# Kernel tuning notes

Hardware: AMD Instinct MI355X
Metric: run time of the kernel (lower is better)

The kernel has to match this reference:

```python
import jax, jax.numpy as jnp
import numpy as np

N = 100000      # nodes
E = 1600000     # edges
IN_DIM = 128    # node_feat_dim
HID = 64        # hidden_dim
K = 3           # Chebyshev order
LAMBDA_MAX = 2.0  # PyG ChebConv default for 'sym' normalization


def setup_inputs():
    key = jax.random.key(0)
    ks = jax.random.split(key, 11)
    x = jax.random.normal(ks[0], (N, IN_DIM), jnp.float32)
    edge_index = jax.random.randint(ks[1], (2, E), 0, N)
    edge_weight = jax.random.uniform(ks[2], (E,), jnp.float32)
    h = jax.random.normal(ks[3], (N, HID), jnp.float32)
    c = jax.random.normal(ks[4], (N, HID), jnp.float32)
    s_in = 1.0 / np.sqrt(IN_DIM)
    s_h = 1.0 / np.sqrt(HID)
    # stacked gate params, order: [input, forget, cell(candidate), output]
    Wx = jax.random.uniform(ks[5], (4, IN_DIM, HID), jnp.float32, -s_in, s_in)
    bg = jax.random.uniform(ks[6], (4, HID), jnp.float32, -s_h, s_h)
    theta = jax.random.uniform(ks[7], (4, K, HID, HID), jnp.float32, -s_h, s_h)
    conv_b = jax.random.uniform(ks[8], (4, HID), jnp.float32, -s_h, s_h)
    Wl = jax.random.uniform(ks[9], (HID, HID), jnp.float32, -s_h, s_h)
    bl = jax.random.uniform(ks[10], (HID,), jnp.float32, -s_h, s_h)
    return dict(x=x, edge_index=edge_index, edge_weight=edge_weight, h=h, c=c,
                Wx=Wx, bg=bg, theta=theta, conv_b=conv_b, Wl=Wl, bl=bl)


def _make_lhat_mm(edge_index, edge_weight, num_nodes, lambda_max):
    # Builds z -> L_hat @ z  with  L_hat = (2/lambda_max) * (I - D^-1/2 A D^-1/2) - I
    src, dst = edge_index[0], edge_index[1]
    w = jnp.where(src == dst, 0.0, edge_weight)  # remove_self_loops
    deg = jax.ops.segment_sum(w, src, num_segments=num_nodes)
    deg_safe = jnp.where(deg > 0, deg, 1.0)
    dinv = jnp.where(deg > 0, jax.lax.rsqrt(deg_safe), 0.0)  # inf -> 0 as in PyG
    lap_w = (2.0 / lambda_max) * (-dinv[src] * w * dinv[dst])  # scaled off-diagonal
    diag = 2.0 / lambda_max - 1.0                              # scaled diag (0 at lmax=2)
    def lhat_mm(z):
        msg = lap_w[:, None] * z[src]                       # [E, HID] gather
        agg = jax.ops.segment_sum(msg, dst, num_segments=num_nodes)
        return agg + diag * z
    return lhat_mm


def reference(x, edge_index, edge_weight, h, c, Wx, bg, theta, conv_b, Wl, bl):
    lhat_mm = _make_lhat_mm(edge_index, edge_weight, x.shape[0], LAMBDA_MAX)
    # Chebyshev basis T_k(L_hat) h ; identical across the 4 gate ChebConvs, so compute once.
    Tx = [h, lhat_mm(h)]
    for _ in range(2, K):
        Tx.append(2.0 * lhat_mm(Tx[-1]) - Tx[-2])
    Tx = jnp.stack(Tx)                                      # [K, N, HID]
    conv = jnp.einsum('knh,gkho->gno', Tx, theta) + conv_b[:, None, :]
    lin = jnp.einsum('nf,gfo->gno', x, Wx) + bg[:, None, :]
    pre = lin + conv                                        # [4, N, HID]
    i = jax.nn.sigmoid(pre[0])
    f = jax.nn.sigmoid(pre[1])
    t = jnp.tanh(pre[2])
    o = jax.nn.sigmoid(pre[3])
    c0 = f * c + i * t
    h0 = o * jnp.tanh(c0)
    out = jax.nn.relu(h0) @ Wl + bl                         # trailing relu + Linear
    return (out, h0, c0)
```

## Files before the change

kernel.cpp:

```cpp
#include <hip/hip_runtime.h>
#include <hip/hip_bf16.h>

#define NN 100000
#define NE 1600000
#define INDIM 128
#define HID 64
#define BSH 9
#define NBUCK 196

typedef __hip_bfloat16 bf16;
typedef unsigned short ushort;
typedef unsigned int uint;
typedef __attribute__((ext_vector_type(8))) short short8;
typedef __attribute__((ext_vector_type(4))) float floatx4;

__device__ __forceinline__ float b2f(bf16 v) { return __bfloat162float(v); }
__device__ __forceinline__ float b2f_raw(ushort u) { return __uint_as_float(((uint)u) << 16); }
__device__ __forceinline__ ushort f2bu(float v) {
    bf16 t = __float2bfloat16(v);
    return *reinterpret_cast<ushort*>(&t);
}
__device__ __forceinline__ float ldin(const void* p, int i, int f32) {
    return f32 ? ((const float*)p)[i] : b2f(((const bf16*)p)[i]);
}
__device__ __forceinline__ float sigmoidf(float x) { return 1.f / (1.f + __expf(-x)); }
__device__ __forceinline__ float tanh_fast(float x) {
    float e = __expf(2.f * x);
    return 1.f - 2.f / (e + 1.f);
}
__device__ __forceinline__ uint4 packf8(const float* f) {
    uint4 u;
    u.x = f2bu(f[0]) | ((uint)f2bu(f[1]) << 16);
    u.y = f2bu(f[2]) | ((uint)f2bu(f[3]) << 16);
    u.z = f2bu(f[4]) | ((uint)f2bu(f[5]) << 16);
    u.w = f2bu(f[6]) | ((uint)f2bu(f[7]) << 16);
    return u;
}
__device__ __forceinline__ uint4 ld8_bf16(const void* p, int off, int f32) {
    if (!f32) return *(const uint4*)((const ushort*)p + off);
    const float* q = (const float*)p + off;
    float4 a = *(const float4*)q, b = *(const float4*)(q + 4);
    float f[8] = {a.x, a.y, a.z, a.w, b.x, b.y, b.z, b.w};
    return packf8(f);
}
__device__ __forceinline__ void ld4w(const void* ew, int e0, int f32, float* w) {
    if (f32) {
        float4 v = *(const float4*)((const float*)ew + e0);
        w[0] = v.x; w[1] = v.y; w[2] = v.z; w[3] = v.w;
    } else {
        uint2 v = *(const uint2*)((const ushort*)ew + e0);
        w[0] = b2f_raw((ushort)(v.x & 0xffff)); w[1] = b2f_raw((ushort)(v.x >> 16));
        w[2] = b2f_raw((ushort)(v.y & 0xffff)); w[3] = b2f_raw((ushort)(v.y >> 16));
    }
}

__global__ void k_sniff(const void* __restrict__ x, int* __restrict__ flag) {
    __shared__ int cnt;
    if (threadIdx.x == 0) cnt = 0;
    __syncthreads();
    const bf16* p = (const bf16*)x;
    int bad = 0;
    for (int i = threadIdx.x; i < 8192; i += 256) {
        float v = b2f(p[i]);
        if (!(fabsf(v) < 1e6f)) bad++;
    }
    atomicAdd(&cnt, bad);
    __syncthreads();
    if (threadIdx.x == 0) flag[0] = (cnt > 32) ? 1 : 0;
}

__global__ __launch_bounds__(256)
void k_count(const int* __restrict__ ei, int* __restrict__ gcntD,
             int* __restrict__ gcntS) {
    __shared__ int hD[NBUCK], hS[NBUCK];
    for (int i = threadIdx.x; i < NBUCK; i += 256) { hD[i] = 0; hS[i] = 0; }
    __syncthreads();
    int e0 = (blockIdx.x * 256 + threadIdx.x) * 16;
    if (e0 < NE) {
        if (e0 + 16 <= NE) {
#pragma unroll
            for (int q = 0; q < 4; q++) {
                int4 s4 = *(const int4*)(ei + e0 + q * 4);
                int4 d4 = *(const int4*)(ei + NE + e0 + q * 4);
                int ss[4] = {s4.x, s4.y, s4.z, s4.w};
                int dd[4] = {d4.x, d4.y, d4.z, d4.w};
#pragma unroll
                for (int j = 0; j < 4; j++)
                    if (ss[j] != dd[j]) {
                        atomicAdd(hD + (dd[j] >> BSH), 1);
                        atomicAdd(hS + (ss[j] >> BSH), 1);
                    }
            }
        } else {
            for (int e = e0; e < NE; e++) {
                int s = ei[e], d = ei[NE + e];
                if (s != d) {
                    atomicAdd(hD + (d >> BSH), 1);
                    atomicAdd(hS + (s >> BSH), 1);
                }
            }
        }
    }
    __syncthreads();
    for (int i = threadIdx.x; i < NBUCK; i += 256) {
        if (hD[i]) atomicAdd(gcntD + i, hD[i]);
        if (hS[i]) atomicAdd(gcntS + i, hS[i]);
    }
}

__global__ __launch_bounds__(256)
void k_scanb(const int* __restrict__ gcntD, const int* __restrict__ gcntS,
             int* __restrict__ bbaseD, int* __restrict__ bbaseS,
             int* __restrict__ gcurD, int* __restrict__ gcurS,
             int* __restrict__ rowptr) {
    __shared__ int sh[256];
    const int t = threadIdx.x;
    int v = (t < NBUCK) ? gcntD[t] : 0;
    sh[t] = v; __syncthreads();
    for (int off = 1; off < 256; off <<= 1) {
        int u = (t >= off) ? sh[t - off] : 0;
        __syncthreads(); sh[t] += u; __syncthreads();
    }
    if (t < NBUCK) { int e = sh[t] - v; bbaseD[t] = e; gcurD[t] = e; }
    if (t == 255) { bbaseD[NBUCK] = sh[255]; rowptr[NN] = sh[255]; }
    __syncthreads();
    int v2 = (t < NBUCK) ? gcntS[t] : 0;
    sh[t] = v2; __syncthreads();
    for (int off = 1; off < 256; off <<= 1) {
        int u = (t >= off) ? sh[t - off] : 0;
        __syncthreads(); sh[t] += u; __syncthreads();
    }
    if (t < NBUCK) { int e = sh[t] - v2; bbaseS[t] = e; gcurS[t] = e; }
    if (t == 255) bbaseS[NBUCK] = sh[255];
}

__global__ __launch_bounds__(256)
void k_part(const int* __restrict__ ei, const void* __restrict__ ew,
            int* __restrict__ gcurD, int* __restrict__ gcurS,
            int2* __restrict__ recD, int2* __restrict__ recS,
            const int* __restrict__ flagp) {
    const int f32 = flagp[0];
    __shared__ int cD[NBUCK], cS[NBUCK], bD[NBUCK], bS[NBUCK];
    for (int i = threadIdx.x; i < NBUCK; i += 256) { cD[i] = 0; cS[i] = 0; }
    __syncthreads();
    const int e0 = (blockIdx.x * 256 + threadIdx.x) * 8;
    int s[8], d[8], rD[8], rS[8];
    float w[8];
    bool act[8];
    if (e0 + 8 <= NE) {
        int4 sa = *(const int4*)(ei + e0), sb = *(const int4*)(ei + e0 + 4);
        int4 da = *(const int4*)(ei + NE + e0), db = *(const int4*)(ei + NE + e0 + 4);
        s[0]=sa.x; s[1]=sa.y; s[2]=sa.z; s[3]=sa.w;
        s[4]=sb.x; s[5]=sb.y; s[6]=sb.z; s[7]=sb.w;
        d[0]=da.x; d[1]=da.y; d[2]=da.z; d[3]=da.w;
        d[4]=db.x; d[5]=db.y; d[6]=db.z; d[7]=db.w;
        ld4w(ew, e0, f32, w); ld4w(ew, e0 + 4, f32, w + 4);
#pragma unroll
        for (int j = 0; j < 8; j++) act[j] = (s[j] != d[j]);
    } else {
#pragma unroll
        for (int j = 0; j < 8; j++) {
            int e = e0 + j;
            if (e < NE) {
                s[j] = ei[e]; d[j] = ei[NE + e]; w[j] = ldin(ew, e, f32);
                act[j] = (s[j] != d[j]);
            } else { s[j] = 0; d[j] = 0; w[j] = 0.f; act[j] = false; }
        }
    }
#pragma unroll
    for (int j = 0; j < 8; j++)
        if (act[j]) {
            rD[j] = atomicAdd(cD + (d[j] >> BSH), 1);
            rS[j] = atomicAdd(cS + (s[j] >> BSH), 1);
        }
    __syncthreads();
    for (int i = threadIdx.x; i < NBUCK; i += 256) {
        bD[i] = cD[i] ? atomicAdd(gcurD + i, cD[i]) : 0;
        bS[i] = cS[i] ? atomicAdd(gcurS + i, cS[i]) : 0;
    }
    __syncthreads();
#pragma unroll
    for (int j = 0; j < 8; j++)
        if (act[j]) {
            int2 pd; pd.x = s[j] | ((d[j] & 511) << 17); pd.y = __float_as_int(w[j]);
            recD[bD[d[j] >> BSH] + rD[j]] = pd;
            int2 ps; ps.x = s[j] & 511; ps.y = __float_as_int(w[j]);
            recS[bS[s[j] >> BSH] + rS[j]] = ps;
        }
}

__global__ __launch_bounds__(512)
void k_build(const int2* __restrict__ recD, const int2* __restrict__ recS,
             const int* __restrict__ bbaseD, const int* __restrict__ bbaseS,
             int* __restrict__ rowptr, int2* __restrict__ csr,
             float* __restrict__ dinv) {
    __shared__ int cnt[512], sh[512], cur[512];
    __shared__ float degf[512];
    const int t = threadIdx.x, b = blockIdx.x;
    cnt[t] = 0; degf[t] = 0.f;
    __syncthreads();
    const int dbase = bbaseD[b], dend = bbaseD[b + 1];
    const int sbase = bbaseS[b], send = bbaseS[b + 1];
    const int nD = dend - dbase, nS = send - sbase;
    const int2* rd = recD + dbase;
    const int2* rs = recS + sbase;
    for (int i = t; i < nD; i += 512) atomicAdd(cnt + (rd[i].x >> 17), 1);
    for (int i = t; i < nS; i += 512) atomicAdd(degf + rs[i].x, __int_as_float(rs[i].y));
    __syncthreads();
    const int own = cnt[t];
    sh[t] = own; __syncthreads();
    for (int off = 1; off < 512; off <<= 1) {
        int u = (t >= off) ? sh[t - off] : 0;
        __syncthreads(); sh[t] += u; __syncthreads();
    }
    const int rstart = dbase + sh[t] - own;
    cur[t] = rstart;
    const int node = (b << BSH) + t;
    if (node < NN) {
        rowptr[node] = rstart;
        float dg = degf[t];
        dinv[node] = dg > 0.f ? rsqrtf(dg) : 0.f;
    }
    __syncthreads();
    for (int i = t; i < nD; i += 512) {
        int2 r = rd[i];
        int pos = atomicAdd(cur + (r.x >> 17), 1);
        int2 o; o.x = r.x & 0x1FFFF; o.y = r.y;
        csr[pos] = o;
    }
}

template<int MODE>
__global__ __launch_bounds__(256)
void k_gath(const int* __restrict__ rowptr, const float* __restrict__ dinv,
            const int2* __restrict__ csr, const void* __restrict__ zin,
            void* __restrict__ outv, const int* __restrict__ flagp) {
    const int f32 = flagp[0];
    int n = (blockIdx.x * 256 + threadIdx.x) >> 6;
    int lane = threadIdx.x & 63;
    if (n >= NN) return;
    int b0 = rowptr[n], e0 = rowptr[n + 1];
    const int2* row = csr + b0;
    int cnt = e0 - b0;
    float acc = 0.f;
    int i = 0;
#define ZLD(sidx) (MODE == 0 ? ldin(zin, (sidx) * 64 + lane, f32) \
                             : b2f_raw(((const ushort*)zin)[(sidx) * 128 + lane]))
    for (; i + 3 < cnt; i += 4) {
        int2 p0 = row[i], p1 = row[i + 1], p2 = row[i + 2], p3 = row[i + 3];
        float z0 = ZLD(p0.x), z1 = ZLD(p1.x), z2 = ZLD(p2.x), z3 = ZLD(p3.x);
        acc = fmaf(dinv[p0.x] * __int_as_float(p0.y), z0, acc);
        acc = fmaf(dinv[p1.x] * __int_as_float(p1.y), z1, acc);
        acc = fmaf(dinv[p2.x] * __int_as_float(p2.y), z2, acc);
        acc = fmaf(dinv[p3.x] * __int_as_float(p3.y), z3, acc);
    }
    for (; i < cnt; i++) {
        int2 p0 = row[i];
        float z0 = ZLD(p0.x);
        acc = fmaf(dinv[p0.x] * __int_as_float(p0.y), z0, acc);
    }
#undef ZLD
    float r = -dinv[n] * acc;
    if (MODE == 0) ((ushort*)outv)[(size_t)n * 128 + lane] = f2bu(r);
    else           ((float*)outv)[(size_t)n * 64 + lane] = r;
}

__global__ void k_wcat(const void* __restrict__ Wx, const void* __restrict__ theta,
                       const void* __restrict__ bg, const void* __restrict__ convb,
                       const void* __restrict__ Wl,
                       ushort* __restrict__ Wf, float* __restrict__ biasP,
                       ushort* __restrict__ WlF, const int* __restrict__ flagp) {
    const int f32 = flagp[0];
    int gid = blockIdx.x * 256 + threadIdx.x;
    if (gid < 81920) {
        int j = gid & 7, l = (gid >> 3) & 63, tile = gid >> 9;
        int kc = tile >> 4, t = tile & 15;
        int r = kc * 32 + ((l >> 4) * 8) + j;
        int g = t & 3;
        int cc = (t >> 2) * 16 + (l & 15);
        float v;
        if (r < 128) {
            v = ldin(Wx, (g * 128 + r) * 64 + cc, f32);
        } else {
            int k3 = (r - 128) >> 6, rr = (r - 128) & 63;
            v = ldin(theta, ((g * 3 + k3) * 64 + rr) * 64 + cc, f32);
        }
        Wf[gid] = f2bu(v);
        if (gid < 256) {
            int o = gid;
            int gg = (o >> 4) & 3;
            int cc2 = (o >> 6) * 16 + (o & 15);
            biasP[o] = ldin(bg, gg * 64 + cc2, f32) + ldin(convb, gg * 64 + cc2, f32);
        }
    } else {
        int gid2 = gid - 81920;
        int j = gid2 & 7, l = (gid2 >> 3) & 63, tile2 = gid2 >> 9;
        int kc2 = tile2 >> 2, t = tile2 & 3;
        int k = kc2 * 32 + ((l >> 4) * 8) + j;
        int n = t * 16 + (l & 15);
        WlF[gid2] = f2bu(ldin(Wl, k * 64 + n, f32));
    }
}

__global__ __launch_bounds__(256)
void k_gates(const void* __restrict__ x, const void* __restrict__ h,
             const void* __restrict__ cin,
             const ushort* __restrict__ Tx1, const float* __restrict__ agg2,
             const ushort* __restrict__ Wf, const float* __restrict__ biasP,
             const ushort* __restrict__ WlF, const void* __restrict__ bl,
             float* __restrict__ outF, float* __restrict__ h0o,
             float* __restrict__ c0o, const int* __restrict__ flagp) {
    const int f32 = flagp[0];
    __shared__ ushort As[4 * 64 * 8];
    __shared__ ushort Hs[64 * 72];
    const int tid = threadIdx.x;
    const int lane = tid & 63;
    const int w = tid >> 6;
    const int base = blockIdx.x * 64;
    const int sm = tid & 63;
    const int skq = tid >> 6;
    const int snode = base + sm;
    const bool svalid = snode < NN;
    uint4* sdst = (uint4*)&As[(((sm >> 4) * 64) + ((sm & 15) + 16 * skq)) * 8];

    floatx4 acc[4][4];
    {
        float bv0 = biasP[w * 64 + 0 * 16 + (lane & 15)];
        float bv1 = biasP[w * 64 + 1 * 16 + (lane & 15)];
        float bv2 = biasP[w * 64 + 2 * 16 + (lane & 15)];
        float bv3 = biasP[w * 64 + 3 * 16 + (lane & 15)];
#pragma unroll
        for (int mt = 0; mt < 4; mt++) {
            acc[mt][0] = (floatx4){bv0, bv0, bv0, bv0};
            acc[mt][1] = (floatx4){bv1, bv1, bv1, bv1};
            acc[mt][2] = (floatx4){bv2, bv2, bv2, bv2};
            acc[mt][3] = (floatx4){bv3, bv3, bv3, bv3};
        }
    }

    for (int kc = 0; kc < 10; kc++) {
        uint4 raw = {0, 0, 0, 0};
        if (svalid) {
            if (kc < 4) {
                raw = ld8_bf16(x, snode * 128 + kc * 32 + skq * 8, f32);
            } else if (kc < 6) {
                raw = ld8_bf16(h, snode * 64 + (kc - 4) * 32 + skq * 8, f32);
            } else if (kc < 8) {
                raw = *(const uint4*)&Tx1[(size_t)snode * 128 + (kc - 6) * 32 + skq * 8];
            } else {
                int off = snode * 64 + (kc - 8) * 32 + skq * 8;
                const float* pa = agg2 + off;
                float4 a = *(const float4*)pa, b = *(const float4*)(pa + 4);
                float av[8] = {a.x, a.y, a.z, a.w, b.x, b.y, b.z, b.w};
                float hv[8];
                if (f32) {
                    const float* ph = (const float*)h + off;
                    float4 h0_ = *(const float4*)ph, h1_ = *(const float4*)(ph + 4);
                    hv[0]=h0_.x; hv[1]=h0_.y; hv[2]=h0_.z; hv[3]=h0_.w;
                    hv[4]=h1_.x; hv[5]=h1_.y; hv[6]=h1_.z; hv[7]=h1_.w;
                } else {
                    uint4 hr = *(const uint4*)((const ushort*)h + off);
                    uint u[4] = {hr.x, hr.y, hr.z, hr.w};
#pragma unroll
                    for (int q = 0; q < 4; q++) {
                        hv[2*q]   = b2f_raw((ushort)(u[q] & 0xffff));
                        hv[2*q+1] = b2f_raw((ushort)(u[q] >> 16));
                    }
                }
                float f[8];
#pragma unroll
                for (int j = 0; j < 8; j++) f[j] = 2.f * av[j] - hv[j];
                raw = packf8(f);
            }
        }
        short8 bF[4];
#pragma unroll
        for (int g = 0; g < 4; g++)
            bF[g] = *(const short8*)&Wf[((kc * 16 + w * 4 + g) * 64 + lane) * 8];

        __syncthreads();
        *sdst = raw;
        __syncthreads();

        short8 aF[4];
#pragma unroll
        for (int mt = 0; mt < 4; mt++)
            aF[mt] = *(const short8*)&As[(mt * 64 + lane) * 8];
#pragma unroll
        for (int mt = 0; mt < 4; mt++)
#pragma unroll
            for (int g = 0; g < 4; g++)
                acc[mt][g] = __builtin_amdgcn_mfma_f32_16x16x32_bf16(
                    aF[mt], bF[g], acc[mt][g], 0, 0, 0);
    }

    const int cc = w * 16 + (lane & 15);
#pragma unroll
    for (int mt = 0; mt < 4; mt++) {
        const int m0 = mt * 16 + ((lane >> 4) * 4);
#pragma unroll
        for (int r = 0; r < 4; r++) {
            int ml = m0 + r;
            int node = base + ml;
            float gi = sigmoidf(acc[mt][0][r]);
            float gf = sigmoidf(acc[mt][1][r]);
            float gt = tanh_fast(acc[mt][2][r]);
            float go = sigmoidf(acc[mt][3][r]);
            float cv = (node < NN) ? ldin(cin, node * 64 + cc, f32) : 0.f;
            float c0 = gf * cv + gi * gt;
            float h0v = go * tanh_fast(c0);
            if (node < NN) {
                c0o[node * 64 + cc] = c0;
                h0o[node * 64 + cc] = h0v;
            }
            Hs[ml * 72 + cc] = f2bu(fmaxf(h0v, 0.f));
        }
    }
    __syncthreads();

    float blv = ldin(bl, w * 16 + (lane & 15), f32);
    floatx4 oacc[4];
#pragma unroll
    for (int mt = 0; mt < 4; mt++) oacc[mt] = (floatx4){blv, blv, blv, blv};
#pragma unroll
    for (int kc2 = 0; kc2 < 2; kc2++) {
        short8 bW = *(const short8*)&WlF[((kc2 * 4 + w) * 64 + lane) * 8];
#pragma unroll
        for (int mt = 0; mt < 4; mt++) {
            short8 aH = *(const short8*)&Hs[(mt * 16 + (lane & 15)) * 72
                                            + kc2 * 32 + (lane >> 4) * 8];
            oacc[mt] = __builtin_amdgcn_mfma_f32_16x16x32_bf16(
                aH, bW, oacc[mt], 0, 0, 0);
        }
    }
#pragma unroll
    for (int mt = 0; mt < 4; mt++) {
        const int m0 = mt * 16 + ((lane >> 4) * 4);
#pragma unroll
        for (int r = 0; r < 4; r++) {
            int node = base + m0 + r;
            if (node < NN)
                outF[node * 64 + w * 16 + (lane & 15)] = oacc[mt][r];
        }
    }
}

extern "C" void kernel_launch(void* const* d_in, const int* in_sizes, int n_in,
                              void* d_out, int out_size, void* d_ws, size_t ws_size,
                              hipStream_t stream) {
    const void* x     = d_in[0];
    const int*  ei    = (const int*)d_in[1];
    const void* ew    = d_in[2];
    const void* h     = d_in[3];
    const void* c     = d_in[4];
    const void* Wx    = d_in[5];
    const void* bg    = d_in[6];
    const void* theta = d_in[7];
    const void* convb = d_in[8];
    const void* Wl    = d_in[9];
    const void* bl    = d_in[10];
    (void)in_sizes; (void)n_in; (void)out_size; (void)ws_size;

    float*  ws     = (float*)d_ws;
    int*    flag   = (int*)ws;
    float*  dinv   = ws + 64;
    int*    rowptr = (int*)(ws + 100064);
    int*    gcntD  = (int*)(ws + 200128);
    int*    gcntS  = (int*)(ws + 200384);
    int*    bbaseD = (int*)(ws + 200640);
    int*    bbaseS = (int*)(ws + 200896);
    int*    gcurD  = (int*)(ws + 201152);
    int*    gcurS  = (int*)(ws + 201408);
    float*  biasP  = ws + 400128;
    ushort* Wf     = (ushort*)(ws + 400384);
    ushort* WlF    = (ushort*)(ws + 441344);

    float* outF = (float*)d_out;
    float* h0o  = outF + (size_t)NN * 64;
    float* c0o  = outF + (size_t)2 * NN * 64;
    ushort* Tx1b = (ushort*)outF;
    float*  agg2 = c0o;
    int2* recD = (int2*)h0o;
    int2* csr  = (int2*)(h0o + 3200000);
    int2* recS = (int2*)c0o;

    k_sniff<<<1, 256, 0, stream>>>(x, flag);
    hipMemsetAsync(gcntD, 0, 512 * 4, stream);

    k_count<<<(NE + 4095) / 4096, 256, 0, stream>>>(ei, gcntD, gcntS);
    k_scanb<<<1, 256, 0, stream>>>(gcntD, gcntS, bbaseD, bbaseS, gcurD, gcurS, rowptr);
    k_part<<<(NE + 2047) / 2048, 256, 0, stream>>>(ei, ew, gcurD, gcurS,
                                                   recD, recS, flag);
    k_build<<<NBUCK, 512, 0, stream>>>(recD, recS, bbaseD, bbaseS,
                                       rowptr, csr, dinv);
    k_wcat<<<336, 256, 0, stream>>>(Wx, theta, bg, convb, Wl, Wf, biasP, WlF, flag);

    k_gath<0><<<25000, 256, 0, stream>>>(rowptr, dinv, csr, h,    Tx1b, flag);
    k_gath<1><<<25000, 256, 0, stream>>>(rowptr, dinv, csr, Tx1b, agg2, flag);

    k_gates<<<(NN + 63) / 64, 256, 0, stream>>>(x, h, c, Tx1b, agg2,
                                                Wf, biasP, WlF, bl,
                                                outF, h0o, c0o, flag);
}
```

Measured before the change: 482.4 us.

## Fuse Chebyshev recurrence into second gather and double-buffer gate GEMM LDS

The second gather kernel now computes T2 = 2*L·T1 - h itself and stores it as bf16, instead of writing fp32 aggregates that the gate kernel later combined with h. This cuts the global write and read traffic for that intermediate and takes the elementwise work out of the gate kernel's load path. Separately, the gate kernel double-buffers its shared-memory A tile and prefetches the next chunk into registers, dropping one barrier per k-step. The cost is extra LDS, a reload of h inside the gather epilogue, and higher register pressure from the prefetch.

```diff
diff --git a/kernel.cpp b/kernel.cpp
--- a/kernel.cpp
+++ b/kernel.cpp
@@ -234,7 +234,8 @@
 __global__ __launch_bounds__(256)
 void k_gath(const int* __restrict__ rowptr, const float* __restrict__ dinv,
             const int2* __restrict__ csr, const void* __restrict__ zin,
-            void* __restrict__ outv, const int* __restrict__ flagp) {
+            const void* __restrict__ hin, ushort* __restrict__ outv,
+            const int* __restrict__ flagp) {
     const int f32 = flagp[0];
     int n = (blockIdx.x * 256 + threadIdx.x) >> 6;
     int lane = threadIdx.x & 63;
@@ -245,7 +246,7 @@
     float acc = 0.f;
     int i = 0;
 #define ZLD(sidx) (MODE == 0 ? ldin(zin, (sidx) * 64 + lane, f32) \
-                             : b2f_raw(((const ushort*)zin)[(sidx) * 128 + lane]))
+                             : b2f_raw(((const ushort*)zin)[(size_t)(sidx) * 128 + lane]))
     for (; i + 3 < cnt; i += 4) {
         int2 p0 = row[i], p1 = row[i + 1], p2 = row[i + 2], p3 = row[i + 3];
         float z0 = ZLD(p0.x), z1 = ZLD(p1.x), z2 = ZLD(p2.x), z3 = ZLD(p3.x);
@@ -261,8 +262,12 @@
     }
 #undef ZLD
     float r = -dinv[n] * acc;
-    if (MODE == 0) ((ushort*)outv)[(size_t)n * 128 + lane] = f2bu(r);
-    else           ((float*)outv)[(size_t)n * 64 + lane] = r;
+    if (MODE == 0) {
+        outv[(size_t)n * 128 + lane] = f2bu(r);
+    } else {
+        float hv = ldin(hin, n * 64 + lane, f32);
+        outv[(size_t)n * 128 + lane] = f2bu(2.f * r - hv);
+    }
 }
 
 __global__ void k_wcat(const void* __restrict__ Wx, const void* __restrict__ theta,
@@ -305,13 +310,13 @@
 __global__ __launch_bounds__(256)
 void k_gates(const void* __restrict__ x, const void* __restrict__ h,
              const void* __restrict__ cin,
-             const ushort* __restrict__ Tx1, const float* __restrict__ agg2,
+             const ushort* __restrict__ Tx1, const ushort* __restrict__ Tx2,
              const ushort* __restrict__ Wf, const float* __restrict__ biasP,
              const ushort* __restrict__ WlF, const void* __restrict__ bl,
              float* __restrict__ outF, float* __restrict__ h0o,
              float* __restrict__ c0o, const int* __restrict__ flagp) {
     const int f32 = flagp[0];
-    __shared__ ushort As[4 * 64 * 8];
+    __shared__ ushort As[2][4 * 64 * 8];
     __shared__ ushort Hs[64 * 72];
     const int tid = threadIdx.x;
     const int lane = tid & 63;
@@ -321,7 +326,7 @@
     const int skq = tid >> 6;
     const int snode = base + sm;
     const bool svalid = snode < NN;
-    uint4* sdst = (uint4*)&As[(((sm >> 4) * 64) + ((sm & 15) + 16 * skq)) * 8];
+    const int soff = (((sm >> 4) * 64) + ((sm & 15) + 16 * skq)) * 8;
 
     floatx4 acc[4][4];
     {
@@ -338,54 +343,31 @@
         }
     }
 
+    auto produce = [&](int kc) -> uint4 {
+        uint4 r = {0, 0, 0, 0};
+        if (!svalid) return r;
+        if (kc < 4)      r = ld8_bf16(x, snode * 128 + kc * 32 + skq * 8, f32);
+        else if (kc < 6) r = ld8_bf16(h, snode * 64 + (kc - 4) * 32 + skq * 8, f32);
+        else if (kc < 8) r = *(const uint4*)&Tx1[(size_t)snode * 128 + (kc - 6) * 32 + skq * 8];
+        else             r = *(const uint4*)&Tx2[(size_t)snode * 128 + (kc - 8) * 32 + skq * 8];
+        return r;
+    };
+
+    uint4 raw = produce(0);
     for (int kc = 0; kc < 10; kc++) {
-        uint4 raw = {0, 0, 0, 0};
-        if (svalid) {
-            if (kc < 4) {
-                raw = ld8_bf16(x, snode * 128 + kc * 32 + skq * 8, f32);
-            } else if (kc < 6) {
-                raw = ld8_bf16(h, snode * 64 + (kc - 4) * 32 + skq * 8, f32);
-            } else if (kc < 8) {
-                raw = *(const uint4*)&Tx1[(size_t)snode * 128 + (kc - 6) * 32 + skq * 8];
-            } else {
-                int off = snode * 64 + (kc - 8) * 32 + skq * 8;
-                const float* pa = agg2 + off;
-                float4 a = *(const float4*)pa, b = *(const float4*)(pa + 4);
-                float av[8] = {a.x, a.y, a.z, a.w, b.x, b.y, b.z, b.w};
-                float hv[8];
-                if (f32) {
-                    const float* ph = (const float*)h + off;
-                    float4 h0_ = *(const float4*)ph, h1_ = *(const float4*)(ph + 4);
-                    hv[0]=h0_.x; hv[1]=h0_.y; hv[2]=h0_.z; hv[3]=h0_.w;
-                    hv[4]=h1_.x; hv[5]=h1_.y; hv[6]=h1_.z; hv[7]=h1_.w;
-                } else {
-                    uint4 hr = *(const uint4*)((const ushort*)h + off);
-                    uint u[4] = {hr.x, hr.y, hr.z, hr.w};
-#pragma unroll
-                    for (int q = 0; q < 4; q++) {
-                        hv[2*q]   = b2f_raw((ushort)(u[q] & 0xffff));
-                        hv[2*q+1] = b2f_raw((ushort)(u[q] >> 16));
-                    }
-                }
-                float f[8];
-#pragma unroll
-                for (int j = 0; j < 8; j++) f[j] = 2.f * av[j] - hv[j];
-                raw = packf8(f);
-            }
-        }
+        *(uint4*)&As[kc & 1][soff] = raw;
+        if (kc < 9) raw = produce(kc + 1);
         short8 bF[4];
 #pragma unroll
         for (int g = 0; g < 4; g++)
             bF[g] = *(const short8*)&Wf[((kc * 16 + w * 4 + g) * 64 + lane) * 8];
 
         __syncthreads();
-        *sdst = raw;
-        __syncthreads();
 
         short8 aF[4];
 #pragma unroll
         for (int mt = 0; mt < 4; mt++)
-            aF[mt] = *(const short8*)&As[(mt * 64 + lane) * 8];
+            aF[mt] = *(const short8*)&As[kc & 1][(mt * 64 + lane) * 8];
 #pragma unroll
         for (int mt = 0; mt < 4; mt++)
 #pragma unroll
@@ -479,7 +461,7 @@
     float* h0o  = outF + (size_t)NN * 64;
     float* c0o  = outF + (size_t)2 * NN * 64;
     ushort* Tx1b = (ushort*)outF;
-    float*  agg2 = c0o;
+    ushort* Tx2b = (ushort*)c0o;
     int2* recD = (int2*)h0o;
     int2* csr  = (int2*)(h0o + 3200000);
     int2* recS = (int2*)c0o;
@@ -495,10 +477,10 @@
                                        rowptr, csr, dinv);
     k_wcat<<<336, 256, 0, stream>>>(Wx, theta, bg, convb, Wl, Wf, biasP, WlF, flag);
 
-    k_gath<0><<<25000, 256, 0, stream>>>(rowptr, dinv, csr, h,    Tx1b, flag);
-    k_gath<1><<<25000, 256, 0, stream>>>(rowptr, dinv, csr, Tx1b, agg2, flag);
-
-    k_gates<<<(NN + 63) / 64, 256, 0, stream>>>(x, h, c, Tx1b, agg2,
+    k_gath<0><<<25000, 256, 0, stream>>>(rowptr, dinv, csr, h,    h, Tx1b, flag);
+    k_gath<1><<<25000, 256, 0, stream>>>(rowptr, dinv, csr, Tx1b, h, Tx2b, flag);
+
+    k_gates<<<(NN + 63) / 64, 256, 0, stream>>>(x, h, c, Tx1b, Tx2b,
                                                 Wf, biasP, WlF, bl,
                                                 outF, h0o, c0o, flag);
 }
```

Result: no change. 478.5 us (-0.8%).
